# Kernel tuning notes

Hardware: AMD Instinct MI355X
Metric: run time of the kernel (lower is better)

Reference implementation:

```python
import jax, jax.numpy as jnp
import numpy as np

NUM_HEADS = 64  # from init_kwargs


def _rx(theta):
    # RX(theta) = [[cos(t/2), -i sin(t/2)], [-i sin(t/2), cos(t/2)]]
    theta = jnp.asarray(theta, jnp.float32)
    c = jnp.cos(theta / 2)
    s = jnp.sin(theta / 2)
    return jnp.stack([jnp.stack([c + 0j, -1j * s], -1),
                      jnp.stack([-1j * s, c + 0j], -1)], -2).astype(jnp.complex64)


def _ry(theta):
    # RY(theta) = [[cos(t/2), -sin(t/2)], [sin(t/2), cos(t/2)]]
    theta = jnp.asarray(theta, jnp.float32)
    c = jnp.cos(theta / 2)
    s = jnp.sin(theta / 2)
    return jnp.stack([jnp.stack([c + 0j, -s + 0j], -1),
                      jnp.stack([s + 0j, c + 0j], -1)], -2).astype(jnp.complex64)


def _apply_1q(state, U, wire):
    # state: (N, 2, 2, ..., 2) with wire w on axis 1+w (torchquantum convention)
    s = jnp.moveaxis(state, 1 + wire, -1)
    if U.ndim == 2:
        s = jnp.einsum('...i,ji->...j', s, U)
    else:  # per-sample gate, U: (N, 2, 2)
        s = jnp.einsum('n...i,nji->n...j', s, U)
    return jnp.moveaxis(s, -1, 1 + wire)


def _cnot(state, c, t):
    s = jnp.moveaxis(state, (1 + c, 1 + t), (-2, -1))
    s = s.at[..., 1, :].set(s[..., 1, ::-1])  # flip target where control==1
    return jnp.moveaxis(s, (-2, -1), (1 + c, 1 + t))


def _qlayer(xf, qparams):
    # xf: (N, d_k) angles; simulates RX-encode, per-wire RY/RX, CNOT ring, PauliZ expvals
    N, dk = xf.shape
    state = jnp.zeros((N, 2 ** dk), jnp.complex64).at[:, 0].set(1.0)
    state = state.reshape((N,) + (2,) * dk)
    for i in range(dk):                      # GeneralEncoder: RX(x_i) on wire i
        state = _apply_1q(state, _rx(xf[:, i]), i)
    for i in range(dk):                      # variational RY, RX per wire
        state = _apply_1q(state, _ry(qparams[i, 0]), i)
        state = _apply_1q(state, _rx(qparams[i, 1]), i)
    for i in range(dk - 1):                  # CNOT chain
        state = _cnot(state, i, i + 1)
    state = _cnot(state, dk - 1, 0)          # ring closure
    probs = state.real ** 2 + state.imag ** 2  # (N, 2,..,2)
    probs = probs.reshape(N, -1)
    # wire w is bit (dk-1-w) of the flattened index (wire 0 = MSB)
    bits = ((jnp.arange(2 ** dk)[:, None] >> jnp.arange(dk - 1, -1, -1)[None, :]) & 1).astype(jnp.float32)
    return probs @ (1.0 - 2.0 * bits)        # (N, dk) PauliZ expectations


def setup_inputs() -> dict:
    key = jax.random.key(0)
    ks = jax.random.split(key, 6)
    B, T, E, dk = 2, 512, 384, 384 // NUM_HEADS
    sc = 1.0 / np.sqrt(E)
    return {
        'x': jax.random.normal(ks[0], (B, T, E), jnp.float32),
        'Wq': jax.random.normal(ks[1], (E, E), jnp.float32) * sc,
        'bq': jnp.zeros((E,), jnp.float32),
        'Wk': jax.random.normal(ks[2], (E, E), jnp.float32) * sc,
        'bk': jnp.zeros((E,), jnp.float32),
        'Wv': jax.random.normal(ks[3], (E, E), jnp.float32) * sc,
        'bv': jnp.zeros((E,), jnp.float32),
        'Wo': jax.random.normal(ks[4], (E, E), jnp.float32) * sc,
        'bo': jnp.zeros((E,), jnp.float32),
        'qparams': jax.random.normal(ks[5], (dk, 2), jnp.float32),
    }


def reference(x, Wq, bq, Wk, bk, Wv, bv, Wo, bo, qparams):
    B, T, E = x.shape
    H = NUM_HEADS
    dk = E // H

    def heads(y):  # (B,T,E) -> (B,H,T,dk)
        return y.reshape(B, T, H, dk).transpose(0, 2, 1, 3)

    q = heads(x @ Wq.T + bq)
    k = heads(x @ Wk.T + bk)
    v = heads(x @ Wv.T + bv)

    def apply_q(layer):
        flat = layer.reshape(-1, dk)
        return _qlayer(flat, qparams).reshape(B, H, T, dk)

    qq, kq, vq = apply_q(q), apply_q(k), apply_q(v)
    scores = jnp.einsum('bhtd,bhsd->bhts', qq, kq) / jnp.sqrt(jnp.float32(dk))
    attn = jax.nn.softmax(scores, axis=-1)
    out = jnp.einsum('bhts,bhsd->bhtd', attn, vq)
    merged = out.transpose(0, 2, 1, 3).reshape(B, T, E)
    return merged @ Wo.T + bo
```

## Files before the change

### kernel.cpp

```cpp
#include <hip/hip_runtime.h>
#include <math.h>

#define SEQ_T   512
#define E_DIM   384
#define H_NUM   64
#define DKQ     6
#define NROWS   1024
#define QKV_ELEMS (NROWS*E_DIM)
#define NCHUNK  4

__device__ __forceinline__ void qmap6(const float* __restrict__ in,
                                      const float* __restrict__ AB,
                                      float* __restrict__ out)
{
    float z[6];
#pragma unroll
    for (int i = 0; i < 6; ++i) {
        float s, c;
        sincosf(in[i], &s, &c);
        z[i] = AB[i] * c - AB[6 + i] * s;
    }
    float z01 = z[0] * z[1];
    float z12 = z[1] * z[2];
    float z34 = z[3] * z[4];
    out[0] = z12 * z34 * z[5];
    out[1] = z01;
    out[2] = z01 * z[2];
    out[3] = out[2] * z[3];
    out[4] = out[3] * z[4];
    out[5] = out[4] * z[5];
}

__device__ __forceinline__ void gemm_32x48(const float* __restrict__ A,
                                           const float* __restrict__ W,
                                           int n0, int e0,
                                           float (&xs)[64][36], float (&ws)[64][52],
                                           float (&acc)[4][6])
{
    const int tid = threadIdx.x;
    const int tx = tid & 7;
    const int ty = tid >> 3;

#pragma unroll
    for (int i = 0; i < 4; ++i)
#pragma unroll
        for (int j = 0; j < 6; ++j) acc[i][j] = 0.f;

    for (int kc = 0; kc < E_DIM; kc += 64) {
#pragma unroll
        for (int w = 0; w < 8; ++w) {
            const int idx = tid + 64 * w;
            const int row = idx & 31;
            const int kf  = idx >> 5;
            const float4 g = *reinterpret_cast<const float4*>(
                A + (size_t)(n0 + row) * E_DIM + kc + kf * 4);
            xs[kf * 4 + 0][row] = g.x;
            xs[kf * 4 + 1][row] = g.y;
            xs[kf * 4 + 2][row] = g.z;
            xs[kf * 4 + 3][row] = g.w;
        }
#pragma unroll
        for (int w = 0; w < 12; ++w) {
            const int idx = tid + 64 * w;
            const int c  = idx % 48;
            const int kf = idx / 48;
            const float4 g = *reinterpret_cast<const float4*>(
                W + (size_t)(e0 + c) * E_DIM + kc + kf * 4);
            ws[kf * 4 + 0][c] = g.x;
            ws[kf * 4 + 1][c] = g.y;
            ws[kf * 4 + 2][c] = g.z;
            ws[kf * 4 + 3][c] = g.w;
        }
        __syncthreads();

#pragma unroll 8
        for (int kk = 0; kk < 64; ++kk) {
            const float4 a = *reinterpret_cast<const float4*>(&xs[kk][ty * 4]);
            const float2 b0 = *reinterpret_cast<const float2*>(&ws[kk][tx * 6 + 0]);
            const float2 b1 = *reinterpret_cast<const float2*>(&ws[kk][tx * 6 + 2]);
            const float2 b2 = *reinterpret_cast<const float2*>(&ws[kk][tx * 6 + 4]);
            const float av[4] = {a.x, a.y, a.z, a.w};
            const float bv[6] = {b0.x, b0.y, b1.x, b1.y, b2.x, b2.y};
#pragma unroll
            for (int i = 0; i < 4; ++i)
#pragma unroll
                for (int j = 0; j < 6; ++j) acc[i][j] += av[i] * bv[j];
        }
        __syncthreads();
    }
}

__global__ __launch_bounds__(64)
void qkv_gemm(const float* __restrict__ x,
              const float* __restrict__ Wq, const float* __restrict__ bq,
              const float* __restrict__ Wk, const float* __restrict__ bk,
              const float* __restrict__ Wv, const float* __restrict__ bv,
              float* __restrict__ qb, float* __restrict__ kb, float* __restrict__ vb)
{
    __shared__ __align__(16) float xs[64][36];
    __shared__ __align__(16) float ws[64][52];

    const int n0 = blockIdx.x * 32;
    const int by = blockIdx.y;
    const int sel = by >> 3;
    const int e0 = (by & 7) * 48;

    const float* W; const float* bias; float* ob;
    if (sel == 0)      { W = Wq; bias = bq; ob = qb; }
    else if (sel == 1) { W = Wk; bias = bk; ob = kb; }
    else               { W = Wv; bias = bv; ob = vb; }

    float acc[4][6];
    gemm_32x48(x, W, n0, e0, xs, ws, acc);

    const int tx = threadIdx.x & 7;
    const int ty = threadIdx.x >> 3;
    const int h = (e0 / 6) + tx;
    const float2 bi0 = *reinterpret_cast<const float2*>(bias + e0 + tx * 6 + 0);
    const float2 bi1 = *reinterpret_cast<const float2*>(bias + e0 + tx * 6 + 2);
    const float2 bi2 = *reinterpret_cast<const float2*>(bias + e0 + tx * 6 + 4);

#pragma unroll
    for (int i = 0; i < 4; ++i) {
        const int n = n0 + ty * 4 + i;
        const int b = n >> 9;
        const int t = n & 511;
        float* rp = ob + (((size_t)(b * H_NUM + h) * SEQ_T) + t) * DKQ;
        float2 w0 = {acc[i][0] + bi0.x, acc[i][1] + bi0.y};
        float2 w1 = {acc[i][2] + bi1.x, acc[i][3] + bi1.y};
        float2 w2 = {acc[i][4] + bi2.x, acc[i][5] + bi2.y};
        *reinterpret_cast<float2*>(rp + 0) = w0;
        *reinterpret_cast<float2*>(rp + 2) = w1;
        *reinterpret_cast<float2*>(rp + 4) = w2;
    }
}

__global__ __launch_bounds__(256)
void qmap_inplace(float* __restrict__ qb, const float* __restrict__ qparams)
{
    const int pid = blockIdx.x * 256 + threadIdx.x;
    float AB[12];
#pragma unroll
    for (int i = 0; i < 6; ++i) {
        const float a = qparams[i * 2 + 0];
        const float b = qparams[i * 2 + 1];
        AB[i]     = cosf(a) * cosf(b);
        AB[6 + i] = sinf(b);
    }
    float4* p = reinterpret_cast<float4*>(qb + (size_t)pid * 12);
    float4 g0 = p[0], g1 = p[1], g2 = p[2];
    float in0[6] = {g0.x, g0.y, g0.z, g0.w, g1.x, g1.y};
    float in1[6] = {g1.z, g1.w, g2.x, g2.y, g2.z, g2.w};
    float o0[6], o1[6];
    qmap6(in0, AB, o0);
    qmap6(in1, AB, o1);
    p[0] = make_float4(o0[0], o0[1], o0[2], o0[3]);
    p[1] = make_float4(o0[4], o0[5], o1[0], o1[1]);
    p[2] = make_float4(o1[2], o1[3], o1[4], o1[5]);
}

__global__ __launch_bounds__(128)
void attn_partial(const float* __restrict__ qb,
                  const float* __restrict__ kb,
                  const float* __restrict__ vb,
                  float* __restrict__ part)
{
    __shared__ __align__(16) float kv[128][12];

    const int bh = blockIdx.x;
    const int c  = blockIdx.y;
    const int t  = threadIdx.x;

    {
        const float* kr = kb + ((size_t)bh * SEQ_T + c * 128 + t) * DKQ;
        const float* vr = vb + ((size_t)bh * SEQ_T + c * 128 + t) * DKQ;
        const float2 k0 = *reinterpret_cast<const float2*>(kr + 0);
        const float2 k1 = *reinterpret_cast<const float2*>(kr + 2);
        const float2 k2 = *reinterpret_cast<const float2*>(kr + 4);
        const float2 v0 = *reinterpret_cast<const float2*>(vr + 0);
        const float2 v1 = *reinterpret_cast<const float2*>(vr + 2);
        const float2 v2 = *reinterpret_cast<const float2*>(vr + 4);
        float4* kvp = reinterpret_cast<float4*>(&kv[t][0]);
        kvp[0] = make_float4(k0.x, k0.y, k1.x, k1.y);
        kvp[1] = make_float4(k2.x, k2.y, v0.x, v0.y);
        kvp[2] = make_float4(v1.x, v1.y, v2.x, v2.y);
    }

    const float inv_sqrt_dk = 0.40824829046386296f;
    float qrow[4][6];
#pragma unroll
    for (int r = 0; r < 4; ++r) {
        const float* qp = qb + ((size_t)bh * SEQ_T + r * 128 + t) * DKQ;
        const float2 q0 = *reinterpret_cast<const float2*>(qp + 0);
        const float2 q1 = *reinterpret_cast<const float2*>(qp + 2);
        const float2 q2 = *reinterpret_cast<const float2*>(qp + 4);
        qrow[r][0] = q0.x * inv_sqrt_dk; qrow[r][1] = q0.y * inv_sqrt_dk;
        qrow[r][2] = q1.x * inv_sqrt_dk; qrow[r][3] = q1.y * inv_sqrt_dk;
        qrow[r][4] = q2.x * inv_sqrt_dk; qrow[r][5] = q2.y * inv_sqrt_dk;
    }
    __syncthreads();

    float accv[4][6];
    float den[4] = {0.f, 0.f, 0.f, 0.f};
#pragma unroll
    for (int r = 0; r < 4; ++r)
#pragma unroll
        for (int d = 0; d < 6; ++d) accv[r][d] = 0.f;

    const float4* kv4 = reinterpret_cast<const float4*>(&kv[0][0]);
#pragma unroll 2
    for (int s = 0; s < 128; ++s) {
        const float4 r0 = kv4[3 * s + 0];
        const float4 r1 = kv4[3 * s + 1];
        const float4 r2 = kv4[3 * s + 2];
#pragma unroll
        for (int r = 0; r < 4; ++r) {
            const float sc = qrow[r][0] * r0.x + qrow[r][1] * r0.y + qrow[r][2] * r0.z
                           + qrow[r][3] * r0.w + qrow[r][4] * r1.x + qrow[r][5] * r1.y;
            const float e = __expf(sc);
            den[r] += e;
            accv[r][0] += e * r1.z; accv[r][1] += e * r1.w;
            accv[r][2] += e * r2.x; accv[r][3] += e * r2.y;
            accv[r][4] += e * r2.z; accv[r][5] += e * r2.w;
        }
    }

#pragma unroll
    for (int r = 0; r < 4; ++r) {
        const int q = r * 128 + t;
        float4* pp = reinterpret_cast<float4*>(
            part + ((size_t)((c * SEQ_T + q) * 128 + bh)) * 8);
        pp[0] = make_float4(accv[r][0], accv[r][1], accv[r][2], accv[r][3]);
        pp[1] = make_float4(accv[r][4], accv[r][5], den[r], 0.f);
    }
}

__global__ __launch_bounds__(256)
void attn_reduce(const float* __restrict__ part, float* __restrict__ merged)
{
    const int idx = blockIdx.x * 256 + threadIdx.x;
    const int bh = idx & 127;
    const int q  = idx >> 7;

    float acc[6] = {0.f, 0.f, 0.f, 0.f, 0.f, 0.f};
    float den = 0.f;
#pragma unroll
    for (int c = 0; c < NCHUNK; ++c) {
        const float4* pp = reinterpret_cast<const float4*>(
            part + ((size_t)((c * SEQ_T + q) * 128 + bh)) * 8);
        const float4 a = pp[0];
        const float4 b = pp[1];
        acc[0] += a.x; acc[1] += a.y; acc[2] += a.z; acc[3] += a.w;
        acc[4] += b.x; acc[5] += b.y; den += b.z;
    }
    const float r = 1.0f / den;
    const int b = bh >> 6;
    const int h = bh & 63;
    float* mp = merged + ((size_t)(b * SEQ_T + q)) * E_DIM + h * DKQ;
    float2 w0 = {acc[0] * r, acc[1] * r};
    float2 w1 = {acc[2] * r, acc[3] * r};
    float2 w2 = {acc[4] * r, acc[5] * r};
    *reinterpret_cast<float2*>(mp + 0) = w0;
    *reinterpret_cast<float2*>(mp + 2) = w1;
    *reinterpret_cast<float2*>(mp + 4) = w2;
}

__global__ __launch_bounds__(64)
void out_gemm(const float* __restrict__ merged,
              const float* __restrict__ Wo, const float* __restrict__ bo,
              float* __restrict__ out)
{
    __shared__ __align__(16) float xs[64][36];
    __shared__ __align__(16) float ws[64][52];

    const int n0 = blockIdx.x * 32;
    const int e0 = blockIdx.y * 48;

    float acc[4][6];
    gemm_32x48(merged, Wo, n0, e0, xs, ws, acc);

    const int tx = threadIdx.x & 7;
    const int ty = threadIdx.x >> 3;
    const float2 bi0 = *reinterpret_cast<const float2*>(bo + e0 + tx * 6 + 0);
    const float2 bi1 = *reinterpret_cast<const float2*>(bo + e0 + tx * 6 + 2);
    const float2 bi2 = *reinterpret_cast<const float2*>(bo + e0 + tx * 6 + 4);

#pragma unroll
    for (int i = 0; i < 4; ++i) {
        const int n = n0 + ty * 4 + i;
        float* rp = out + (size_t)n * E_DIM + e0 + tx * 6;
        float2 w0 = {acc[i][0] + bi0.x, acc[i][1] + bi0.y};
        float2 w1 = {acc[i][2] + bi1.x, acc[i][3] + bi1.y};
        float2 w2 = {acc[i][4] + bi2.x, acc[i][5] + bi2.y};
        *reinterpret_cast<float2*>(rp + 0) = w0;
        *reinterpret_cast<float2*>(rp + 2) = w1;
        *reinterpret_cast<float2*>(rp + 4) = w2;
    }
}

extern "C" void kernel_launch(void* const* d_in, const int* in_sizes, int n_in,
                              void* d_out, int out_size, void* d_ws, size_t ws_size,
                              hipStream_t stream)
{
    const float* x  = (const float*)d_in[0];
    const float* Wq = (const float*)d_in[1];
    const float* bq = (const float*)d_in[2];
    const float* Wk = (const float*)d_in[3];
    const float* bk = (const float*)d_in[4];
    const float* Wv = (const float*)d_in[5];
    const float* bv = (const float*)d_in[6];
    const float* Wo = (const float*)d_in[7];
    const float* bo = (const float*)d_in[8];
    const float* qp = (const float*)d_in[9];
    float* out = (float*)d_out;

    float* qb     = (float*)d_ws;
    float* kb     = qb + QKV_ELEMS;
    float* vb     = kb + QKV_ELEMS;
    float* merged = vb + QKV_ELEMS;
    float* part   = merged + QKV_ELEMS;

    qkv_gemm<<<dim3(32, 24), 64, 0, stream>>>(x, Wq, bq, Wk, bk, Wv, bv, qb, kb, vb);
    qmap_inplace<<<384, 256, 0, stream>>>(qb, qp);
    attn_partial<<<dim3(128, NCHUNK), 128, 0, stream>>>(qb, kb, vb, part);
    attn_reduce<<<256, 256, 0, stream>>>(part, merged);
    out_gemm<<<dim3(32, 8), 64, 0, stream>>>(merged, Wo, bo, out);
}
```

Before: 166.7 us.

## Fuse all stages into one cooperative persistent kernel with grid syncs

Replaces the five-kernel pipeline with a single cooperatively launched kernel of 256 blocks. It runs the QKV GEMM, attention partials, reduction and output GEMM as phases separated by grid-wide syncs, and keeps the old kernels as a fallback if the cooperative launch fails. The quantum map and the 1/sqrt(dk) scaling on Q move into the QKV GEMM epilogue, which removes the separate in-place pass over q/k/v. GEMM tiles grow to 64x96 per 256-thread block. This cuts launch gaps and one global round trip, but the GEMM phases use fewer blocks (192 and 64) and each grid sync adds a barrier cost.

```diff
diff --git a/kernel.cpp b/kernel.cpp
--- a/kernel.cpp
+++ b/kernel.cpp
@@ -1,5 +1,8 @@
 #include <hip/hip_runtime.h>
+#include <hip/hip_cooperative_groups.h>
 #include <math.h>
+
+namespace cg = cooperative_groups;
 
 #define SEQ_T   512
 #define E_DIM   384
@@ -8,6 +11,7 @@
 #define NROWS   1024
 #define QKV_ELEMS (NROWS*E_DIM)
 #define NCHUNK  4
+#define INV_SQRT6 0.40824829046386296f
 
 __device__ __forceinline__ void qmap6(const float* __restrict__ in,
                                       const float* __restrict__ AB,
@@ -31,16 +35,351 @@
     out[5] = out[4] * z[5];
 }
 
-__device__ __forceinline__ void gemm_32x48(const float* __restrict__ A,
-                                           const float* __restrict__ W,
-                                           int n0, int e0,
-                                           float (&xs)[64][36], float (&ws)[64][52],
-                                           float (&acc)[4][6])
-{
+__global__ __launch_bounds__(256)
+void mega_kernel(const float* __restrict__ x,
+                 const float* __restrict__ Wq, const float* __restrict__ bq,
+                 const float* __restrict__ Wk, const float* __restrict__ bk,
+                 const float* __restrict__ Wv, const float* __restrict__ bv,
+                 const float* __restrict__ Wo, const float* __restrict__ bo,
+                 const float* __restrict__ qparams,
+                 float* __restrict__ qb, float* __restrict__ kb, float* __restrict__ vb,
+                 float* __restrict__ part, float* __restrict__ merged,
+                 float* __restrict__ out)
+{
+    __shared__ __align__(16) float xs[64][68];
+    __shared__ __align__(16) float ws[64][100];
+    __shared__ __align__(16) float kv[2][128][12];
+
+    cg::grid_group grid = cg::this_grid();
+
+    const int tid  = threadIdx.x;
+    const int lane = tid & 63;
+    const int wid  = tid >> 6;
+    const int bid  = blockIdx.x;
+
+    if (bid < 192) {
+        const int bx = bid & 15;
+        const int by = bid >> 4;
+        const int n0 = bx * 64;
+        const int sel = by >> 2;
+        const int e0 = (by & 3) * 96;
+
+        const float* W; const float* bias; float* ob;
+        if (sel == 0)      { W = Wq; bias = bq; ob = qb; }
+        else if (sel == 1) { W = Wk; bias = bk; ob = kb; }
+        else               { W = Wv; bias = bv; ob = vb; }
+
+        float AB[12];
+#pragma unroll
+        for (int i = 0; i < 6; ++i) {
+            const float a = qparams[i * 2 + 0];
+            const float b = qparams[i * 2 + 1];
+            AB[i]     = cosf(a) * cosf(b);
+            AB[6 + i] = sinf(b);
+        }
+
+        float acc[4][6];
+#pragma unroll
+        for (int i = 0; i < 4; ++i)
+#pragma unroll
+            for (int j = 0; j < 6; ++j) acc[i][j] = 0.f;
+
+        const int wr = (wid >> 1) * 32;
+        const int wc = (wid & 1) * 48;
+        const int tx = lane & 7;
+        const int ty = lane >> 3;
+
+        for (int kc = 0; kc < E_DIM; kc += 64) {
+#pragma unroll
+            for (int w = 0; w < 4; ++w) {
+                const int idx = tid + 256 * w;
+                const int row = idx & 63;
+                const int kf  = idx >> 6;
+                const float4 g = *reinterpret_cast<const float4*>(
+                    x + (size_t)(n0 + row) * E_DIM + kc + kf * 4);
+                xs[kf * 4 + 0][row] = g.x;
+                xs[kf * 4 + 1][row] = g.y;
+                xs[kf * 4 + 2][row] = g.z;
+                xs[kf * 4 + 3][row] = g.w;
+            }
+#pragma unroll
+            for (int w = 0; w < 6; ++w) {
+                const int idx = tid + 256 * w;
+                const int c  = idx % 96;
+                const int kf = idx / 96;
+                const float4 g = *reinterpret_cast<const float4*>(
+                    W + (size_t)(e0 + c) * E_DIM + kc + kf * 4);
+                ws[kf * 4 + 0][c] = g.x;
+                ws[kf * 4 + 1][c] = g.y;
+                ws[kf * 4 + 2][c] = g.z;
+                ws[kf * 4 + 3][c] = g.w;
+            }
+            __syncthreads();
+#pragma unroll 8
+            for (int kk = 0; kk < 64; ++kk) {
+                const float4 a = *reinterpret_cast<const float4*>(&xs[kk][wr + ty * 4]);
+                const float2 b0 = *reinterpret_cast<const float2*>(&ws[kk][wc + tx * 6 + 0]);
+                const float2 b1 = *reinterpret_cast<const float2*>(&ws[kk][wc + tx * 6 + 2]);
+                const float2 b2 = *reinterpret_cast<const float2*>(&ws[kk][wc + tx * 6 + 4]);
+                const float av[4] = {a.x, a.y, a.z, a.w};
+                const float bv6[6] = {b0.x, b0.y, b1.x, b1.y, b2.x, b2.y};
+#pragma unroll
+                for (int i = 0; i < 4; ++i)
+#pragma unroll
+                    for (int j = 0; j < 6; ++j) acc[i][j] += av[i] * bv6[j];
+            }
+            __syncthreads();
+        }
+
+        const int h = (e0 + wc) / 6 + tx;
+        const float2 bi0 = *reinterpret_cast<const float2*>(bias + e0 + wc + tx * 6 + 0);
+        const float2 bi1 = *reinterpret_cast<const float2*>(bias + e0 + wc + tx * 6 + 2);
+        const float2 bi2 = *reinterpret_cast<const float2*>(bias + e0 + wc + tx * 6 + 4);
+        const float qs = (sel == 0) ? INV_SQRT6 : 1.0f;
+#pragma unroll
+        for (int i = 0; i < 4; ++i) {
+            const int n = n0 + wr + ty * 4 + i;
+            const int b = n >> 9;
+            const int t = n & 511;
+            float y[6] = {acc[i][0] + bi0.x, acc[i][1] + bi0.y,
+                          acc[i][2] + bi1.x, acc[i][3] + bi1.y,
+                          acc[i][4] + bi2.x, acc[i][5] + bi2.y};
+            float o[6];
+            qmap6(y, AB, o);
+            float* rp = ob + (((size_t)(b * H_NUM + h) * SEQ_T) + t) * DKQ;
+            float2 w0 = {o[0] * qs, o[1] * qs};
+            float2 w1 = {o[2] * qs, o[3] * qs};
+            float2 w2 = {o[4] * qs, o[5] * qs};
+            *reinterpret_cast<float2*>(rp + 0) = w0;
+            *reinterpret_cast<float2*>(rp + 2) = w1;
+            *reinterpret_cast<float2*>(rp + 4) = w2;
+        }
+    }
+    grid.sync();
+
+    {
+        const int group = tid >> 7;
+        const int t = tid & 127;
+        const int pair = bid * 2 + group;
+        const int bh = pair >> 2;
+        const int c  = pair & 3;
+
+        {
+            const float* kr = kb + ((size_t)bh * SEQ_T + c * 128 + t) * DKQ;
+            const float* vr = vb + ((size_t)bh * SEQ_T + c * 128 + t) * DKQ;
+            const float2 k0 = *reinterpret_cast<const float2*>(kr + 0);
+            const float2 k1 = *reinterpret_cast<const float2*>(kr + 2);
+            const float2 k2 = *reinterpret_cast<const float2*>(kr + 4);
+            const float2 v0 = *reinterpret_cast<const float2*>(vr + 0);
+            const float2 v1 = *reinterpret_cast<const float2*>(vr + 2);
+            const float2 v2 = *reinterpret_cast<const float2*>(vr + 4);
+            float4* kvp = reinterpret_cast<float4*>(&kv[group][t][0]);
+            kvp[0] = make_float4(k0.x, k0.y, k1.x, k1.y);
+            kvp[1] = make_float4(k2.x, k2.y, v0.x, v0.y);
+            kvp[2] = make_float4(v1.x, v1.y, v2.x, v2.y);
+        }
+
+        float qrow[4][6];
+#pragma unroll
+        for (int r = 0; r < 4; ++r) {
+            const float* qp2 = qb + ((size_t)bh * SEQ_T + r * 128 + t) * DKQ;
+            const float2 q0 = *reinterpret_cast<const float2*>(qp2 + 0);
+            const float2 q1 = *reinterpret_cast<const float2*>(qp2 + 2);
+            const float2 q2 = *reinterpret_cast<const float2*>(qp2 + 4);
+            qrow[r][0] = q0.x; qrow[r][1] = q0.y;
+            qrow[r][2] = q1.x; qrow[r][3] = q1.y;
+            qrow[r][4] = q2.x; qrow[r][5] = q2.y;
+        }
+        __syncthreads();
+
+        float accv[4][6];
+        float den[4] = {0.f, 0.f, 0.f, 0.f};
+#pragma unroll
+        for (int r = 0; r < 4; ++r)
+#pragma unroll
+            for (int d = 0; d < 6; ++d) accv[r][d] = 0.f;
+
+        const float4* kv4 = reinterpret_cast<const float4*>(&kv[group][0][0]);
+#pragma unroll 2
+        for (int s = 0; s < 128; ++s) {
+            const float4 r0 = kv4[3 * s + 0];
+            const float4 r1 = kv4[3 * s + 1];
+            const float4 r2 = kv4[3 * s + 2];
+#pragma unroll
+            for (int r = 0; r < 4; ++r) {
+                const float sc = qrow[r][0] * r0.x + qrow[r][1] * r0.y + qrow[r][2] * r0.z
+                               + qrow[r][3] * r0.w + qrow[r][4] * r1.x + qrow[r][5] * r1.y;
+                const float e = __expf(sc);
+                den[r] += e;
+                accv[r][0] += e * r1.z; accv[r][1] += e * r1.w;
+                accv[r][2] += e * r2.x; accv[r][3] += e * r2.y;
+                accv[r][4] += e * r2.z; accv[r][5] += e * r2.w;
+            }
+        }
+
+#pragma unroll
+        for (int r = 0; r < 4; ++r) {
+            const int q = r * 128 + t;
+            float4* pp = reinterpret_cast<float4*>(
+                part + ((size_t)((c * SEQ_T + q) * 128 + bh)) * 8);
+            pp[0] = make_float4(accv[r][0], accv[r][1], accv[r][2], accv[r][3]);
+            pp[1] = make_float4(accv[r][4], accv[r][5], den[r], 0.f);
+        }
+    }
+    grid.sync();
+
+    {
+        const int idx = bid * 256 + tid;
+        const int bh = idx & 127;
+        const int q  = idx >> 7;
+
+        float acc6[6] = {0.f, 0.f, 0.f, 0.f, 0.f, 0.f};
+        float den = 0.f;
+#pragma unroll
+        for (int c = 0; c < NCHUNK; ++c) {
+            const float4* pp = reinterpret_cast<const float4*>(
+                part + ((size_t)((c * SEQ_T + q) * 128 + bh)) * 8);
+            const float4 a = pp[0];
+            const float4 b = pp[1];
+            acc6[0] += a.x; acc6[1] += a.y; acc6[2] += a.z; acc6[3] += a.w;
+            acc6[4] += b.x; acc6[5] += b.y; den += b.z;
+        }
+        const float r = 1.0f / den;
+        const int b = bh >> 6;
+        const int h = bh & 63;
+        float* mp = merged + ((size_t)(b * SEQ_T + q)) * E_DIM + h * DKQ;
+        float2 w0 = {acc6[0] * r, acc6[1] * r};
+        float2 w1 = {acc6[2] * r, acc6[3] * r};
+        float2 w2 = {acc6[4] * r, acc6[5] * r};
+        *reinterpret_cast<float2*>(mp + 0) = w0;
+        *reinterpret_cast<float2*>(mp + 2) = w1;
+        *reinterpret_cast<float2*>(mp + 4) = w2;
+    }
+    grid.sync();
+
+    if (bid < 64) {
+        const int bx = bid & 15;
+        const int ey = bid >> 4;
+        const int n0 = bx * 64;
+        const int e0 = ey * 96;
+
+        float acc[4][6];
+#pragma unroll
+        for (int i = 0; i < 4; ++i)
+#pragma unroll
+            for (int j = 0; j < 6; ++j) acc[i][j] = 0.f;
+
+        const int wr = (wid >> 1) * 32;
+        const int wc = (wid & 1) * 48;
+        const int tx = lane & 7;
+        const int ty = lane >> 3;
+
+        for (int kc = 0; kc < E_DIM; kc += 64) {
+#pragma unroll
+            for (int w = 0; w < 4; ++w) {
+                const int idx = tid + 256 * w;
+                const int row = idx & 63;
+                const int kf  = idx >> 6;
+                const float4 g = *reinterpret_cast<const float4*>(
+                    merged + (size_t)(n0 + row) * E_DIM + kc + kf * 4);
+                xs[kf * 4 + 0][row] = g.x;
+                xs[kf * 4 + 1][row] = g.y;
+                xs[kf * 4 + 2][row] = g.z;
+                xs[kf * 4 + 3][row] = g.w;
+            }
+#pragma unroll
+            for (int w = 0; w < 6; ++w) {
+                const int idx = tid + 256 * w;
+                const int c  = idx % 96;
+                const int kf = idx / 96;
+                const float4 g = *reinterpret_cast<const float4*>(
+                    Wo + (size_t)(e0 + c) * E_DIM + kc + kf * 4);
+                ws[kf * 4 + 0][c] = g.x;
+                ws[kf * 4 + 1][c] = g.y;
+                ws[kf * 4 + 2][c] = g.z;
+                ws[kf * 4 + 3][c] = g.w;
+            }
+            __syncthreads();
+#pragma unroll 8
+            for (int kk = 0; kk < 64; ++kk) {
+                const float4 a = *reinterpret_cast<const float4*>(&xs[kk][wr + ty * 4]);
+                const float2 b0 = *reinterpret_cast<const float2*>(&ws[kk][wc + tx * 6 + 0]);
+                const float2 b1 = *reinterpret_cast<const float2*>(&ws[kk][wc + tx * 6 + 2]);
+                const float2 b2 = *reinterpret_cast<const float2*>(&ws[kk][wc + tx * 6 + 4]);
+                const float av[4] = {a.x, a.y, a.z, a.w};
+                const float bv6[6] = {b0.x, b0.y, b1.x, b1.y, b2.x, b2.y};
+#pragma unroll
+                for (int i = 0; i < 4; ++i)
+#pragma unroll
+                    for (int j = 0; j < 6; ++j) acc[i][j] += av[i] * bv6[j];
+            }
+            __syncthreads();
+        }
+
+        const float2 bi0 = *reinterpret_cast<const float2*>(bo + e0 + wc + tx * 6 + 0);
+        const float2 bi1 = *reinterpret_cast<const float2*>(bo + e0 + wc + tx * 6 + 2);
+        const float2 bi2 = *reinterpret_cast<const float2*>(bo + e0 + wc + tx * 6 + 4);
+#pragma unroll
+        for (int i = 0; i < 4; ++i) {
+            const int n = n0 + wr + ty * 4 + i;
+            float* rp = out + (size_t)n * E_DIM + e0 + wc + tx * 6;
+            float2 w0 = {acc[i][0] + bi0.x, acc[i][1] + bi0.y};
+            float2 w1 = {acc[i][2] + bi1.x, acc[i][3] + bi1.y};
+            float2 w2 = {acc[i][4] + bi2.x, acc[i][5] + bi2.y};
+            *reinterpret_cast<float2*>(rp + 0) = w0;
+            *reinterpret_cast<float2*>(rp + 2) = w1;
+            *reinterpret_cast<float2*>(rp + 4) = w2;
+        }
+    }
+}
+
+__global__ __launch_bounds__(256)
+void qmap_inplace(float* __restrict__ qb, const float* __restrict__ qparams)
+{
+    const int pid = blockIdx.x * 256 + threadIdx.x;
+    float AB[12];
+#pragma unroll
+    for (int i = 0; i < 6; ++i) {
+        const float a = qparams[i * 2 + 0];
+        const float b = qparams[i * 2 + 1];
+        AB[i]     = cosf(a) * cosf(b);
+        AB[6 + i] = sinf(b);
+    }
+    float4* p = reinterpret_cast<float4*>(qb + (size_t)pid * 12);
+    float4 g0 = p[0], g1 = p[1], g2 = p[2];
+    float in0[6] = {g0.x, g0.y, g0.z, g0.w, g1.x, g1.y};
+    float in1[6] = {g1.z, g1.w, g2.x, g2.y, g2.z, g2.w};
+    float o0[6], o1[6];
+    qmap6(in0, AB, o0);
+    qmap6(in1, AB, o1);
+    p[0] = make_float4(o0[0], o0[1], o0[2], o0[3]);
+    p[1] = make_float4(o0[4], o0[5], o1[0], o1[1]);
+    p[2] = make_float4(o1[2], o1[3], o1[4], o1[5]);
+}
+
+__global__ __launch_bounds__(64)
+void fb_qkv_gemm(const float* __restrict__ x,
+                 const float* __restrict__ Wq, const float* __restrict__ bq,
+                 const float* __restrict__ Wk, const float* __restrict__ bk,
+                 const float* __restrict__ Wv, const float* __restrict__ bv,
+                 float* __restrict__ qb, float* __restrict__ kb, float* __restrict__ vb)
+{
+    __shared__ __align__(16) float xs[64][36];
+    __shared__ __align__(16) float ws[64][52];
     const int tid = threadIdx.x;
     const int tx = tid & 7;
     const int ty = tid >> 3;
-
+    const int n0 = blockIdx.x * 32;
+    const int by = blockIdx.y;
+    const int sel = by >> 3;
+    const int e0 = (by & 7) * 48;
+
+    const float* W; const float* bias; float* ob;
+    if (sel == 0)      { W = Wq; bias = bq; ob = qb; }
+    else if (sel == 1) { W = Wk; bias = bk; ob = kb; }
+    else               { W = Wv; bias = bv; ob = vb; }
+
+    float acc[4][6];
 #pragma unroll
     for (int i = 0; i < 4; ++i)
 #pragma unroll
@@ -53,11 +392,9 @@
             const int row = idx & 31;
             const int kf  = idx >> 5;
             const float4 g = *reinterpret_cast<const float4*>(
-                A + (size_t)(n0 + row) * E_DIM + kc + kf * 4);
-            xs[kf * 4 + 0][row] = g.x;
-            xs[kf * 4 + 1][row] = g.y;
-            xs[kf * 4 + 2][row] = g.z;
-            xs[kf * 4 + 3][row] = g.w;
+                x + (size_t)(n0 + row) * E_DIM + kc + kf * 4);
+            xs[kf * 4 + 0][row] = g.x; xs[kf * 4 + 1][row] = g.y;
+            xs[kf * 4 + 2][row] = g.z; xs[kf * 4 + 3][row] = g.w;
         }
 #pragma unroll
         for (int w = 0; w < 12; ++w) {
@@ -66,13 +403,10 @@
             const int kf = idx / 48;
             const float4 g = *reinterpret_cast<const float4*>(
                 W + (size_t)(e0 + c) * E_DIM + kc + kf * 4);
-            ws[kf * 4 + 0][c] = g.x;
-            ws[kf * 4 + 1][c] = g.y;
-            ws[kf * 4 + 2][c] = g.z;
-            ws[kf * 4 + 3][c] = g.w;
+            ws[kf * 4 + 0][c] = g.x; ws[kf * 4 + 1][c] = g.y;
+            ws[kf * 4 + 2][c] = g.z; ws[kf * 4 + 3][c] = g.w;
         }
         __syncthreads();
-
 #pragma unroll 8
         for (int kk = 0; kk < 64; ++kk) {
             const float4 a = *reinterpret_cast<const float4*>(&xs[kk][ty * 4]);
@@ -80,46 +414,19 @@
             const float2 b1 = *reinterpret_cast<const float2*>(&ws[kk][tx * 6 + 2]);
             const float2 b2 = *reinterpret_cast<const float2*>(&ws[kk][tx * 6 + 4]);
             const float av[4] = {a.x, a.y, a.z, a.w};
-            const float bv[6] = {b0.x, b0.y, b1.x, b1.y, b2.x, b2.y};
+            const float bv6[6] = {b0.x, b0.y, b1.x, b1.y, b2.x, b2.y};
 #pragma unroll
             for (int i = 0; i < 4; ++i)
 #pragma unroll
-                for (int j = 0; j < 6; ++j) acc[i][j] += av[i] * bv[j];
+                for (int j = 0; j < 6; ++j) acc[i][j] += av[i] * bv6[j];
         }
         __syncthreads();
     }
-}
-
-__global__ __launch_bounds__(64)
-void qkv_gemm(const float* __restrict__ x,
-              const float* __restrict__ Wq, const float* __restrict__ bq,
-              const float* __restrict__ Wk, const float* __restrict__ bk,
-              const float* __restrict__ Wv, const float* __restrict__ bv,
-              float* __restrict__ qb, float* __restrict__ kb, float* __restrict__ vb)
-{
-    __shared__ __align__(16) float xs[64][36];
-    __shared__ __align__(16) float ws[64][52];
-
-    const int n0 = blockIdx.x * 32;
-    const int by = blockIdx.y;
-    const int sel = by >> 3;
-    const int e0 = (by & 7) * 48;
-
-    const float* W; const float* bias; float* ob;
-    if (sel == 0)      { W = Wq; bias = bq; ob = qb; }
-    else if (sel == 1) { W = Wk; bias = bk; ob = kb; }
-    else               { W = Wv; bias = bv; ob = vb; }
-
-    float acc[4][6];
-    gemm_32x48(x, W, n0, e0, xs, ws, acc);
-
-    const int tx = threadIdx.x & 7;
-    const int ty = threadIdx.x >> 3;
+
     const int h = (e0 / 6) + tx;
     const float2 bi0 = *reinterpret_cast<const float2*>(bias + e0 + tx * 6 + 0);
     const float2 bi1 = *reinterpret_cast<const float2*>(bias + e0 + tx * 6 + 2);
     const float2 bi2 = *reinterpret_cast<const float2*>(bias + e0 + tx * 6 + 4);
-
 #pragma unroll
     for (int i = 0; i < 4; ++i) {
         const int n = n0 + ty * 4 + i;
@@ -135,42 +442,16 @@
     }
 }
 
-__global__ __launch_bounds__(256)
-void qmap_inplace(float* __restrict__ qb, const float* __restrict__ qparams)
-{
-    const int pid = blockIdx.x * 256 + threadIdx.x;
-    float AB[12];
-#pragma unroll
-    for (int i = 0; i < 6; ++i) {
-        const float a = qparams[i * 2 + 0];
-        const float b = qparams[i * 2 + 1];
-        AB[i]     = cosf(a) * cosf(b);
-        AB[6 + i] = sinf(b);
-    }
-    float4* p = reinterpret_cast<float4*>(qb + (size_t)pid * 12);
-    float4 g0 = p[0], g1 = p[1], g2 = p[2];
-    float in0[6] = {g0.x, g0.y, g0.z, g0.w, g1.x, g1.y};
-    float in1[6] = {g1.z, g1.w, g2.x, g2.y, g2.z, g2.w};
-    float o0[6], o1[6];
-    qmap6(in0, AB, o0);
-    qmap6(in1, AB, o1);
-    p[0] = make_float4(o0[0], o0[1], o0[2], o0[3]);
-    p[1] = make_float4(o0[4], o0[5], o1[0], o1[1]);
-    p[2] = make_float4(o1[2], o1[3], o1[4], o1[5]);
-}
-
 __global__ __launch_bounds__(128)
-void attn_partial(const float* __restrict__ qb,
-                  const float* __restrict__ kb,
-                  const float* __restrict__ vb,
-                  float* __restrict__ part)
+void fb_attn_partial(const float* __restrict__ qb,
+                     const float* __restrict__ kb,
+                     const float* __restrict__ vb,
+                     float* __restrict__ part)
 {
     __shared__ __align__(16) float kv[128][12];
-
     const int bh = blockIdx.x;
     const int c  = blockIdx.y;
     const int t  = threadIdx.x;
-
     {
         const float* kr = kb + ((size_t)bh * SEQ_T + c * 128 + t) * DKQ;
         const float* vr = vb + ((size_t)bh * SEQ_T + c * 128 + t) * DKQ;
@@ -185,8 +466,7 @@
         kvp[1] = make_float4(k2.x, k2.y, v0.x, v0.y);
         kvp[2] = make_float4(v1.x, v1.y, v2.x, v2.y);
     }
-
-    const float inv_sqrt_dk = 0.40824829046386296f;
+    const float inv = INV_SQRT6;
     float qrow[4][6];
 #pragma unroll
     for (int r = 0; r < 4; ++r) {
@@ -194,19 +474,17 @@
         const float2 q0 = *reinterpret_cast<const float2*>(qp + 0);
         const float2 q1 = *reinterpret_cast<const float2*>(qp + 2);
         const float2 q2 = *reinterpret_cast<const float2*>(qp + 4);
-        qrow[r][0] = q0.x * inv_sqrt_dk; qrow[r][1] = q0.y * inv_sqrt_dk;
-        qrow[r][2] = q1.x * inv_sqrt_dk; qrow[r][3] = q1.y * inv_sqrt_dk;
-        qrow[r][4] = q2.x * inv_sqrt_dk; qrow[r][5] = q2.y * inv_sqrt_dk;
+        qrow[r][0] = q0.x * inv; qrow[r][1] = q0.y * inv;
+        qrow[r][2] = q1.x * inv; qrow[r][3] = q1.y * inv;
+        qrow[r][4] = q2.x * inv; qrow[r][5] = q2.y * inv;
     }
     __syncthreads();
-
     float accv[4][6];
     float den[4] = {0.f, 0.f, 0.f, 0.f};
 #pragma unroll
     for (int r = 0; r < 4; ++r)
 #pragma unroll
         for (int d = 0; d < 6; ++d) accv[r][d] = 0.f;
-
     const float4* kv4 = reinterpret_cast<const float4*>(&kv[0][0]);
 #pragma unroll 2
     for (int s = 0; s < 128; ++s) {
@@ -224,7 +502,6 @@
             accv[r][4] += e * r2.z; accv[r][5] += e * r2.w;
         }
     }
-
 #pragma unroll
     for (int r = 0; r < 4; ++r) {
         const int q = r * 128 + t;
@@ -236,12 +513,11 @@
 }
 
 __global__ __launch_bounds__(256)
-void attn_reduce(const float* __restrict__ part, float* __restrict__ merged)
+void fb_attn_reduce(const float* __restrict__ part, float* __restrict__ merged)
 {
     const int idx = blockIdx.x * 256 + threadIdx.x;
     const int bh = idx & 127;
     const int q  = idx >> 7;
-
     float acc[6] = {0.f, 0.f, 0.f, 0.f, 0.f, 0.f};
     float den = 0.f;
 #pragma unroll
@@ -266,25 +542,65 @@
 }
 
 __global__ __launch_bounds__(64)
-void out_gemm(const float* __restrict__ merged,
-              const float* __restrict__ Wo, const float* __restrict__ bo,
-              float* __restrict__ out)
+void fb_out_gemm(const float* __restrict__ merged,
+                 const float* __restrict__ Wo, const float* __restrict__ bo,
+                 float* __restrict__ out)
 {
     __shared__ __align__(16) float xs[64][36];
     __shared__ __align__(16) float ws[64][52];
-
+    const int tid = threadIdx.x;
+    const int tx = tid & 7;
+    const int ty = tid >> 3;
     const int n0 = blockIdx.x * 32;
     const int e0 = blockIdx.y * 48;
 
     float acc[4][6];
-    gemm_32x48(merged, Wo, n0, e0, xs, ws, acc);
-
-    const int tx = threadIdx.x & 7;
-    const int ty = threadIdx.x >> 3;
+#pragma unroll
+    for (int i = 0; i < 4; ++i)
+#pragma unroll
+        for (int j = 0; j < 6; ++j) acc[i][j] = 0.f;
+
+    for (int kc = 0; kc < E_DIM; kc += 64) {
+#pragma unroll
+        for (int w = 0; w < 8; ++w) {
+            const int idx = tid + 64 * w;
+            const int row = idx & 31;
+            const int kf  = idx >> 5;
+            const float4 g = *reinterpret_cast<const float4*>(
+                merged + (size_t)(n0 + row) * E_DIM + kc + kf * 4);
+            xs[kf * 4 + 0][row] = g.x; xs[kf * 4 + 1][row] = g.y;
+            xs[kf * 4 + 2][row] = g.z; xs[kf * 4 + 3][row] = g.w;
+        }
+#pragma unroll
+        for (int w = 0; w < 12; ++w) {
+            const int idx = tid + 64 * w;
+            const int c  = idx % 48;
+            const int kf = idx / 48;
+            const float4 g = *reinterpret_cast<const float4*>(
+                Wo + (size_t)(e0 + c) * E_DIM + kc + kf * 4);
+            ws[kf * 4 + 0][c] = g.x; ws[kf * 4 + 1][c] = g.y;
+            ws[kf * 4 + 2][c] = g.z; ws[kf * 4 + 3][c] = g.w;
+        }
+        __syncthreads();
+#pragma unroll 8
+        for (int kk = 0; kk < 64; ++kk) {
+            const float4 a = *reinterpret_cast<const float4*>(&xs[kk][ty * 4]);
+            const float2 b0 = *reinterpret_cast<const float2*>(&ws[kk][tx * 6 + 0]);
+            const float2 b1 = *reinterpret_cast<const float2*>(&ws[kk][tx * 6 + 2]);
+            const float2 b2 = *reinterpret_cast<const float2*>(&ws[kk][tx * 6 + 4]);
+            const float av[4] = {a.x, a.y, a.z, a.w};
+            const float bv6[6] = {b0.x, b0.y, b1.x, b1.y, b2.x, b2.y};
+#pragma unroll
+            for (int i = 0; i < 4; ++i)
+#pragma unroll
+                for (int j = 0; j < 6; ++j) acc[i][j] += av[i] * bv6[j];
+        }
+        __syncthreads();
+    }
+
     const float2 bi0 = *reinterpret_cast<const float2*>(bo + e0 + tx * 6 + 0);
     const float2 bi1 = *reinterpret_cast<const float2*>(bo + e0 + tx * 6 + 2);
     const float2 bi2 = *reinterpret_cast<const float2*>(bo + e0 + tx * 6 + 4);
-
 #pragma unroll
     for (int i = 0; i < 4; ++i) {
         const int n = n0 + ty * 4 + i;
@@ -320,9 +636,18 @@
     float* merged = vb + QKV_ELEMS;
     float* part   = merged + QKV_ELEMS;
 
-    qkv_gemm<<<dim3(32, 24), 64, 0, stream>>>(x, Wq, bq, Wk, bk, Wv, bv, qb, kb, vb);
-    qmap_inplace<<<384, 256, 0, stream>>>(qb, qp);
-    attn_partial<<<dim3(128, NCHUNK), 128, 0, stream>>>(qb, kb, vb, part);
-    attn_reduce<<<256, 256, 0, stream>>>(part, merged);
-    out_gemm<<<dim3(32, 8), 64, 0, stream>>>(merged, Wo, bo, out);
-}
+    void* args[] = {(void*)&x, (void*)&Wq, (void*)&bq, (void*)&Wk, (void*)&bk,
+                    (void*)&Wv, (void*)&bv, (void*)&Wo, (void*)&bo, (void*)&qp,
+                    (void*)&qb, (void*)&kb, (void*)&vb, (void*)&part,
+                    (void*)&merged, (void*)&out};
+    hipError_t err = hipLaunchCooperativeKernel((const void*)mega_kernel,
+                                                dim3(256), dim3(256),
+                                                args, 0, stream);
+    if (err != hipSuccess) {
+        fb_qkv_gemm<<<dim3(32, 24), 64, 0, stream>>>(x, Wq, bq, Wk, bk, Wv, bv, qb, kb, vb);
+        qmap_inplace<<<384, 256, 0, stream>>>(qb, qp);
+        fb_attn_partial<<<dim3(128, NCHUNK), 128, 0, stream>>>(qb, kb, vb, part);
+        fb_attn_reduce<<<256, 256, 0, stream>>>(part, merged);
+        fb_out_gemm<<<dim3(32, 8), 64, 0, stream>>>(merged, Wo, bo, out);
+    }
+}
```

Measured after the change: 276.6 us. 1.66x slower.

## Fuse qmap into QKV GEMM epilogue and attention reduce into output GEMM

Applied to the files above, without the earlier changes.

Applies the quantum feature map and the 1/sqrt(dk) scale for q inside the QKV GEMM epilogue, removing a separate read-modify-write pass. The cross-chunk attention reduction and softmax normalisation now happen in the output GEMM prologue, which builds the merged tile in shared memory from the partials. This removes two kernel launches and the merged intermediate buffer. In exchange, every column block of the output GEMM recomputes the same reduction with strided partial reads, and the large shared-memory tile lowers occupancy.

```diff
diff --git a/kernel.cpp b/kernel.cpp
--- a/kernel.cpp
+++ b/kernel.cpp
@@ -8,6 +8,7 @@
 #define NROWS   1024
 #define QKV_ELEMS (NROWS*E_DIM)
 #define NCHUNK  4
+#define INV_SQRT6 0.40824829046386296f
 
 __device__ __forceinline__ void qmap6(const float* __restrict__ in,
                                       const float* __restrict__ AB,
@@ -31,16 +32,30 @@
     out[5] = out[4] * z[5];
 }
 
-__device__ __forceinline__ void gemm_32x48(const float* __restrict__ A,
-                                           const float* __restrict__ W,
-                                           int n0, int e0,
-                                           float (&xs)[64][36], float (&ws)[64][52],
-                                           float (&acc)[4][6])
-{
+__global__ __launch_bounds__(64)
+void qkv_gemm_qmap(const float* __restrict__ x,
+                   const float* __restrict__ Wq, const float* __restrict__ bq,
+                   const float* __restrict__ Wk, const float* __restrict__ bk,
+                   const float* __restrict__ Wv, const float* __restrict__ bv,
+                   const float* __restrict__ qparams,
+                   float* __restrict__ qb, float* __restrict__ kb, float* __restrict__ vb)
+{
+    __shared__ __align__(16) float xs[64][36];
+    __shared__ __align__(16) float ws[64][52];
     const int tid = threadIdx.x;
     const int tx = tid & 7;
     const int ty = tid >> 3;
-
+    const int n0 = blockIdx.x * 32;
+    const int by = blockIdx.y;
+    const int sel = by >> 3;
+    const int e0 = (by & 7) * 48;
+
+    const float* W; const float* bias; float* ob;
+    if (sel == 0)      { W = Wq; bias = bq; ob = qb; }
+    else if (sel == 1) { W = Wk; bias = bk; ob = kb; }
+    else               { W = Wv; bias = bv; ob = vb; }
+
+    float acc[4][6];
 #pragma unroll
     for (int i = 0; i < 4; ++i)
 #pragma unroll
@@ -53,11 +68,9 @@
             const int row = idx & 31;
             const int kf  = idx >> 5;
             const float4 g = *reinterpret_cast<const float4*>(
-                A + (size_t)(n0 + row) * E_DIM + kc + kf * 4);
-            xs[kf * 4 + 0][row] = g.x;
-            xs[kf * 4 + 1][row] = g.y;
-            xs[kf * 4 + 2][row] = g.z;
-            xs[kf * 4 + 3][row] = g.w;
+                x + (size_t)(n0 + row) * E_DIM + kc + kf * 4);
+            xs[kf * 4 + 0][row] = g.x; xs[kf * 4 + 1][row] = g.y;
+            xs[kf * 4 + 2][row] = g.z; xs[kf * 4 + 3][row] = g.w;
         }
 #pragma unroll
         for (int w = 0; w < 12; ++w) {
@@ -66,13 +79,10 @@
             const int kf = idx / 48;
             const float4 g = *reinterpret_cast<const float4*>(
                 W + (size_t)(e0 + c) * E_DIM + kc + kf * 4);
-            ws[kf * 4 + 0][c] = g.x;
-            ws[kf * 4 + 1][c] = g.y;
-            ws[kf * 4 + 2][c] = g.z;
-            ws[kf * 4 + 3][c] = g.w;
+            ws[kf * 4 + 0][c] = g.x; ws[kf * 4 + 1][c] = g.y;
+            ws[kf * 4 + 2][c] = g.z; ws[kf * 4 + 3][c] = g.w;
         }
         __syncthreads();
-
 #pragma unroll 8
         for (int kk = 0; kk < 64; ++kk) {
             const float4 a = *reinterpret_cast<const float4*>(&xs[kk][ty * 4]);
@@ -80,65 +90,15 @@
             const float2 b1 = *reinterpret_cast<const float2*>(&ws[kk][tx * 6 + 2]);
             const float2 b2 = *reinterpret_cast<const float2*>(&ws[kk][tx * 6 + 4]);
             const float av[4] = {a.x, a.y, a.z, a.w};
-            const float bv[6] = {b0.x, b0.y, b1.x, b1.y, b2.x, b2.y};
+            const float bv6[6] = {b0.x, b0.y, b1.x, b1.y, b2.x, b2.y};
 #pragma unroll
             for (int i = 0; i < 4; ++i)
 #pragma unroll
-                for (int j = 0; j < 6; ++j) acc[i][j] += av[i] * bv[j];
+                for (int j = 0; j < 6; ++j) acc[i][j] += av[i] * bv6[j];
         }
         __syncthreads();
     }
-}
-
-__global__ __launch_bounds__(64)
-void qkv_gemm(const float* __restrict__ x,
-              const float* __restrict__ Wq, const float* __restrict__ bq,
-              const float* __restrict__ Wk, const float* __restrict__ bk,
-              const float* __restrict__ Wv, const float* __restrict__ bv,
-              float* __restrict__ qb, float* __restrict__ kb, float* __restrict__ vb)
-{
-    __shared__ __align__(16) float xs[64][36];
-    __shared__ __align__(16) float ws[64][52];
-
-    const int n0 = blockIdx.x * 32;
-    const int by = blockIdx.y;
-    const int sel = by >> 3;
-    const int e0 = (by & 7) * 48;
-
-    const float* W; const float* bias; float* ob;
-    if (sel == 0)      { W = Wq; bias = bq; ob = qb; }
-    else if (sel == 1) { W = Wk; bias = bk; ob = kb; }
-    else               { W = Wv; bias = bv; ob = vb; }
-
-    float acc[4][6];
-    gemm_32x48(x, W, n0, e0, xs, ws, acc);
-
-    const int tx = threadIdx.x & 7;
-    const int ty = threadIdx.x >> 3;
-    const int h = (e0 / 6) + tx;
-    const float2 bi0 = *reinterpret_cast<const float2*>(bias + e0 + tx * 6 + 0);
-    const float2 bi1 = *reinterpret_cast<const float2*>(bias + e0 + tx * 6 + 2);
-    const float2 bi2 = *reinterpret_cast<const float2*>(bias + e0 + tx * 6 + 4);
-
-#pragma unroll
-    for (int i = 0; i < 4; ++i) {
-        const int n = n0 + ty * 4 + i;
-        const int b = n >> 9;
-        const int t = n & 511;
-        float* rp = ob + (((size_t)(b * H_NUM + h) * SEQ_T) + t) * DKQ;
-        float2 w0 = {acc[i][0] + bi0.x, acc[i][1] + bi0.y};
-        float2 w1 = {acc[i][2] + bi1.x, acc[i][3] + bi1.y};
-        float2 w2 = {acc[i][4] + bi2.x, acc[i][5] + bi2.y};
-        *reinterpret_cast<float2*>(rp + 0) = w0;
-        *reinterpret_cast<float2*>(rp + 2) = w1;
-        *reinterpret_cast<float2*>(rp + 4) = w2;
-    }
-}
-
-__global__ __launch_bounds__(256)
-void qmap_inplace(float* __restrict__ qb, const float* __restrict__ qparams)
-{
-    const int pid = blockIdx.x * 256 + threadIdx.x;
+
     float AB[12];
 #pragma unroll
     for (int i = 0; i < 6; ++i) {
@@ -147,16 +107,29 @@
         AB[i]     = cosf(a) * cosf(b);
         AB[6 + i] = sinf(b);
     }
-    float4* p = reinterpret_cast<float4*>(qb + (size_t)pid * 12);
-    float4 g0 = p[0], g1 = p[1], g2 = p[2];
-    float in0[6] = {g0.x, g0.y, g0.z, g0.w, g1.x, g1.y};
-    float in1[6] = {g1.z, g1.w, g2.x, g2.y, g2.z, g2.w};
-    float o0[6], o1[6];
-    qmap6(in0, AB, o0);
-    qmap6(in1, AB, o1);
-    p[0] = make_float4(o0[0], o0[1], o0[2], o0[3]);
-    p[1] = make_float4(o0[4], o0[5], o1[0], o1[1]);
-    p[2] = make_float4(o1[2], o1[3], o1[4], o1[5]);
+    const int h = (e0 / 6) + tx;
+    const float2 bi0 = *reinterpret_cast<const float2*>(bias + e0 + tx * 6 + 0);
+    const float2 bi1 = *reinterpret_cast<const float2*>(bias + e0 + tx * 6 + 2);
+    const float2 bi2 = *reinterpret_cast<const float2*>(bias + e0 + tx * 6 + 4);
+    const float qs = (sel == 0) ? INV_SQRT6 : 1.0f;
+#pragma unroll
+    for (int i = 0; i < 4; ++i) {
+        const int n = n0 + ty * 4 + i;
+        const int b = n >> 9;
+        const int t = n & 511;
+        float y[6] = {acc[i][0] + bi0.x, acc[i][1] + bi0.y,
+                      acc[i][2] + bi1.x, acc[i][3] + bi1.y,
+                      acc[i][4] + bi2.x, acc[i][5] + bi2.y};
+        float o[6];
+        qmap6(y, AB, o);
+        float* rp = ob + (((size_t)(b * H_NUM + h) * SEQ_T) + t) * DKQ;
+        float2 w0 = {o[0] * qs, o[1] * qs};
+        float2 w1 = {o[2] * qs, o[3] * qs};
+        float2 w2 = {o[4] * qs, o[5] * qs};
+        *reinterpret_cast<float2*>(rp + 0) = w0;
+        *reinterpret_cast<float2*>(rp + 2) = w1;
+        *reinterpret_cast<float2*>(rp + 4) = w2;
+    }
 }
 
 __global__ __launch_bounds__(128)
@@ -166,11 +139,9 @@
                   float* __restrict__ part)
 {
     __shared__ __align__(16) float kv[128][12];
-
     const int bh = blockIdx.x;
     const int c  = blockIdx.y;
     const int t  = threadIdx.x;
-
     {
         const float* kr = kb + ((size_t)bh * SEQ_T + c * 128 + t) * DKQ;
         const float* vr = vb + ((size_t)bh * SEQ_T + c * 128 + t) * DKQ;
@@ -185,8 +156,6 @@
         kvp[1] = make_float4(k2.x, k2.y, v0.x, v0.y);
         kvp[2] = make_float4(v1.x, v1.y, v2.x, v2.y);
     }
-
-    const float inv_sqrt_dk = 0.40824829046386296f;
     float qrow[4][6];
 #pragma unroll
     for (int r = 0; r < 4; ++r) {
@@ -194,19 +163,17 @@
         const float2 q0 = *reinterpret_cast<const float2*>(qp + 0);
         const float2 q1 = *reinterpret_cast<const float2*>(qp + 2);
         const float2 q2 = *reinterpret_cast<const float2*>(qp + 4);
-        qrow[r][0] = q0.x * inv_sqrt_dk; qrow[r][1] = q0.y * inv_sqrt_dk;
-        qrow[r][2] = q1.x * inv_sqrt_dk; qrow[r][3] = q1.y * inv_sqrt_dk;
-        qrow[r][4] = q2.x * inv_sqrt_dk; qrow[r][5] = q2.y * inv_sqrt_dk;
+        qrow[r][0] = q0.x; qrow[r][1] = q0.y;
+        qrow[r][2] = q1.x; qrow[r][3] = q1.y;
+        qrow[r][4] = q2.x; qrow[r][5] = q2.y;
     }
     __syncthreads();
-
     float accv[4][6];
     float den[4] = {0.f, 0.f, 0.f, 0.f};
 #pragma unroll
     for (int r = 0; r < 4; ++r)
 #pragma unroll
         for (int d = 0; d < 6; ++d) accv[r][d] = 0.f;
-
     const float4* kv4 = reinterpret_cast<const float4*>(&kv[0][0]);
 #pragma unroll 2
     for (int s = 0; s < 128; ++s) {
@@ -224,7 +191,6 @@
             accv[r][4] += e * r2.z; accv[r][5] += e * r2.w;
         }
     }
-
 #pragma unroll
     for (int r = 0; r < 4; ++r) {
         const int q = r * 128 + t;
@@ -235,56 +201,89 @@
     }
 }
 
-__global__ __launch_bounds__(256)
-void attn_reduce(const float* __restrict__ part, float* __restrict__ merged)
-{
-    const int idx = blockIdx.x * 256 + threadIdx.x;
-    const int bh = idx & 127;
-    const int q  = idx >> 7;
-
-    float acc[6] = {0.f, 0.f, 0.f, 0.f, 0.f, 0.f};
-    float den = 0.f;
-#pragma unroll
-    for (int c = 0; c < NCHUNK; ++c) {
-        const float4* pp = reinterpret_cast<const float4*>(
-            part + ((size_t)((c * SEQ_T + q) * 128 + bh)) * 8);
-        const float4 a = pp[0];
-        const float4 b = pp[1];
-        acc[0] += a.x; acc[1] += a.y; acc[2] += a.z; acc[3] += a.w;
-        acc[4] += b.x; acc[5] += b.y; den += b.z;
-    }
-    const float r = 1.0f / den;
-    const int b = bh >> 6;
-    const int h = bh & 63;
-    float* mp = merged + ((size_t)(b * SEQ_T + q)) * E_DIM + h * DKQ;
-    float2 w0 = {acc[0] * r, acc[1] * r};
-    float2 w1 = {acc[2] * r, acc[3] * r};
-    float2 w2 = {acc[4] * r, acc[5] * r};
-    *reinterpret_cast<float2*>(mp + 0) = w0;
-    *reinterpret_cast<float2*>(mp + 2) = w1;
-    *reinterpret_cast<float2*>(mp + 4) = w2;
-}
-
 __global__ __launch_bounds__(64)
-void out_gemm(const float* __restrict__ merged,
-              const float* __restrict__ Wo, const float* __restrict__ bo,
-              float* __restrict__ out)
-{
-    __shared__ __align__(16) float xs[64][36];
+void out_gemm_fused(const float* __restrict__ part,
+                    const float* __restrict__ Wo, const float* __restrict__ bo,
+                    float* __restrict__ out)
+{
+    __shared__ float deninv[32][65];
+    __shared__ float amg[32][385];
     __shared__ __align__(16) float ws[64][52];
 
+    const int tid = threadIdx.x;
+    const int tx = tid & 7;
+    const int ty = tid >> 3;
     const int n0 = blockIdx.x * 32;
     const int e0 = blockIdx.y * 48;
+    const int b  = n0 >> 9;
+    const int q0 = n0 & 511;
+
+#pragma unroll 4
+    for (int i = 0; i < 32; ++i) {
+        float den = 0.f;
+#pragma unroll
+        for (int c = 0; c < NCHUNK; ++c)
+            den += part[((size_t)((c * SEQ_T + q0 + i) * 128) + b * H_NUM + tid) * 8 + 6];
+        deninv[i][tid] = 1.0f / den;
+    }
+    __syncthreads();
+
+#pragma unroll 4
+    for (int i = 0; i < 192; ++i) {
+        const int idx = tid + 64 * i;
+        const int k   = idx % E_DIM;
+        const int row = idx / E_DIM;
+        const int h = k / 6;
+        const int d = k - h * 6;
+        float s = 0.f;
+#pragma unroll
+        for (int c = 0; c < NCHUNK; ++c)
+            s += part[((size_t)((c * SEQ_T + q0 + row) * 128) + b * H_NUM + h) * 8 + d];
+        amg[row][k] = s * deninv[row][h];
+    }
+    __syncthreads();
 
     float acc[4][6];
-    gemm_32x48(merged, Wo, n0, e0, xs, ws, acc);
-
-    const int tx = threadIdx.x & 7;
-    const int ty = threadIdx.x >> 3;
+#pragma unroll
+    for (int i = 0; i < 4; ++i)
+#pragma unroll
+        for (int j = 0; j < 6; ++j) acc[i][j] = 0.f;
+
+    for (int kc = 0; kc < E_DIM; kc += 64) {
+#pragma unroll
+        for (int w = 0; w < 12; ++w) {
+            const int idx = tid + 64 * w;
+            const int c  = idx % 48;
+            const int kf = idx / 48;
+            const float4 g = *reinterpret_cast<const float4*>(
+                Wo + (size_t)(e0 + c) * E_DIM + kc + kf * 4);
+            ws[kf * 4 + 0][c] = g.x; ws[kf * 4 + 1][c] = g.y;
+            ws[kf * 4 + 2][c] = g.z; ws[kf * 4 + 3][c] = g.w;
+        }
+        __syncthreads();
+#pragma unroll 8
+        for (int kk = 0; kk < 64; ++kk) {
+            const int k = kc + kk;
+            const float a0 = amg[ty * 4 + 0][k];
+            const float a1 = amg[ty * 4 + 1][k];
+            const float a2 = amg[ty * 4 + 2][k];
+            const float a3 = amg[ty * 4 + 3][k];
+            const float2 b0 = *reinterpret_cast<const float2*>(&ws[kk][tx * 6 + 0]);
+            const float2 b1 = *reinterpret_cast<const float2*>(&ws[kk][tx * 6 + 2]);
+            const float2 b2 = *reinterpret_cast<const float2*>(&ws[kk][tx * 6 + 4]);
+            const float av[4] = {a0, a1, a2, a3};
+            const float bv6[6] = {b0.x, b0.y, b1.x, b1.y, b2.x, b2.y};
+#pragma unroll
+            for (int i = 0; i < 4; ++i)
+#pragma unroll
+                for (int j = 0; j < 6; ++j) acc[i][j] += av[i] * bv6[j];
+        }
+        __syncthreads();
+    }
+
     const float2 bi0 = *reinterpret_cast<const float2*>(bo + e0 + tx * 6 + 0);
     const float2 bi1 = *reinterpret_cast<const float2*>(bo + e0 + tx * 6 + 2);
     const float2 bi2 = *reinterpret_cast<const float2*>(bo + e0 + tx * 6 + 4);
-
 #pragma unroll
     for (int i = 0; i < 4; ++i) {
         const int n = n0 + ty * 4 + i;
@@ -314,15 +313,12 @@
     const float* qp = (const float*)d_in[9];
     float* out = (float*)d_out;
 
-    float* qb     = (float*)d_ws;
-    float* kb     = qb + QKV_ELEMS;
-    float* vb     = kb + QKV_ELEMS;
-    float* merged = vb + QKV_ELEMS;
-    float* part   = merged + QKV_ELEMS;
-
-    qkv_gemm<<<dim3(32, 24), 64, 0, stream>>>(x, Wq, bq, Wk, bk, Wv, bv, qb, kb, vb);
-    qmap_inplace<<<384, 256, 0, stream>>>(qb, qp);
+    float* qb   = (float*)d_ws;
+    float* kb   = qb + QKV_ELEMS;
+    float* vb   = kb + QKV_ELEMS;
+    float* part = vb + QKV_ELEMS;
+
+    qkv_gemm_qmap<<<dim3(32, 24), 64, 0, stream>>>(x, Wq, bq, Wk, bk, Wv, bv, qp, qb, kb, vb);
     attn_partial<<<dim3(128, NCHUNK), 128, 0, stream>>>(qb, kb, vb, part);
-    attn_reduce<<<256, 256, 0, stream>>>(part, merged);
-    out_gemm<<<dim3(32, 8), 64, 0, stream>>>(merged, Wo, bo, out);
-}
+    out_gemm_fused<<<dim3(32, 8), 64, 0, stream>>>(part, Wo, bo, out);
+}
```

Measured after the change: 184.2 us. 1.1x slower.
